# Optimization experiments

Hardware: AMD Instinct MI355X
Metric: run time of the kernel (lower is better)

Reference implementation:

```python
import jax, jax.numpy as jnp
import numpy as np

B, M, N, K = 8192, 512, 2048, 16
P = 50      # top-k support size per iteration
EPS = 0.01


def soft_threshold(x, theta, p):
    # x: [B, N]
    if p == 0:
        return jnp.sign(x) * jax.nn.relu(jnp.abs(x) - theta)
    abs_ = jnp.abs(x)
    topk_vals, _ = jax.lax.top_k(abs_, p)          # sorted descending
    thresh = topk_vals[:, -1]                      # min of top-k, per row
    keep = (abs_ > thresh[:, None]).astype(x.dtype)
    shrunk = jnp.sign(x) * jax.nn.relu(abs_ - theta)
    return keep * x + (1.0 - keep) * shrunk


def setup_inputs() -> dict:
    key = jax.random.key(0)
    k_y, k_A = jax.random.split(key)
    y = jax.random.normal(k_y, (B, M), dtype=jnp.float32)
    A = jax.random.normal(k_A, (M, N), dtype=jnp.float32) / np.sqrt(M)
    gamma = jnp.full((K,), 3.0, dtype=jnp.float32)
    theta = jnp.full((K,), 0.02, dtype=jnp.float32)
    a_param = jnp.full((K,), 0.01, dtype=jnp.float32)
    v = jnp.ones((K,), dtype=jnp.float32)
    vu = jnp.full((K,), 0.05, dtype=jnp.float32)
    theta_init = jnp.float32(1.0)
    return {"y": y, "A": A, "gamma": gamma, "theta": theta,
            "a_param": a_param, "v": v, "vu": vu,
            "theta_init": theta_init, "info": 0}


def reference(y, A, gamma, theta, a_param, v, vu, theta_init, info):
    # forward_op(x)  = x @ A.T   : [B,N] -> [B,M]
    # backward_op(b) = b @ A     : [B,M] -> [B,N]
    x = jnp.zeros((y.shape[0], A.shape[1]), dtype=y.dtype)
    for i in range(K):
        t = theta_init if i == 0 else theta[i]
        gain = 1.0 + t * vu[i] * jnp.exp(-v[i] * jnp.abs(x))
        b = (gain * x) @ A.T - y                 # residual in measurement space
        c = b @ A                                # gradient step direction
        x_new = soft_threshold(x - gamma[i] * c, theta[i], P)
        overshoot = 1.0 + a_param[i] / (jnp.abs(x_new - x) + EPS)
        x = overshoot * x_new + (1.0 - overshoot) * x
    return (x, jnp.zeros((K, 1), dtype=y.dtype), jnp.zeros((K, 1), dtype=y.dtype))
```

## Files before the change

kernel.cpp:

```cpp
#include <hip/hip_runtime.h>
#include <math.h>

#define Bsz  8192
#define Mdim 512
#define Ndim 2048
#define Kit  16
#define Pk   50
#define EPSv 0.01f

typedef __attribute__((ext_vector_type(8))) short bf16x8;
typedef __attribute__((ext_vector_type(4))) float f32x4;

static __device__ __forceinline__ unsigned short f2bf(float f) {
    unsigned u = __float_as_uint(f);
    return (unsigned short)((u + 0x7fffu + ((u >> 16) & 1u)) >> 16);
}
static __device__ __forceinline__ float bf2f(unsigned short h) {
    return __uint_as_float(((unsigned)h) << 16);
}

static __device__ __forceinline__ void gl16(const void* g, void* l) {
    __builtin_amdgcn_global_load_lds(
        (const __attribute__((address_space(1))) unsigned int*)g,
        (__attribute__((address_space(3))) unsigned int*)l, 16, 0, 0);
}

#define PIPE_BARRIER() __builtin_amdgcn_s_barrier()

#define MFMA3(acc_, bh_, bl_, ah_, al_)                                         \
    acc_ = __builtin_amdgcn_mfma_f32_16x16x32_bf16(bh_, ah_, acc_, 0, 0, 0);    \
    acc_ = __builtin_amdgcn_mfma_f32_16x16x32_bf16(bh_, al_, acc_, 0, 0, 0);    \
    acc_ = __builtin_amdgcn_mfma_f32_16x16x32_bf16(bl_, ah_, acc_, 0, 0, 0);

__global__ __launch_bounds__(256) void presplit_A(
    const float* __restrict__ A, unsigned short* __restrict__ Ah,
    unsigned short* __restrict__ Al, unsigned short* __restrict__ AhT,
    unsigned short* __restrict__ AlT)
{
    int idx = blockIdx.x * 256 + threadIdx.x;
    int m = idx >> 11, n = idx & (Ndim - 1);
    float a = A[idx];
    unsigned short h = f2bf(a);
    unsigned short l = f2bf(a - bf2f(h));
    Ah[idx] = h; Al[idx] = l;
    AhT[(size_t)n * Mdim + m] = h;
    AlT[(size_t)n * Mdim + m] = l;
}

__global__ __launch_bounds__(256) void split_negy_kernel(const float* __restrict__ y,
                                                         unsigned short* __restrict__ bS) {
    int i = blockIdx.x * 256 + threadIdx.x;
    float4 v = ((const float4*)y)[i];
    int idx = i * 4;
    int r = idx >> 9, c = idx & 511;
    float f0 = -v.x, f1 = -v.y, f2 = -v.z, f3 = -v.w;
    unsigned short h0 = f2bf(f0), h1 = f2bf(f1), h2 = f2bf(f2), h3 = f2bf(f3);
    ushort4 hv = make_ushort4(h0, h1, h2, h3);
    ushort4 lv = make_ushort4(f2bf(f0 - bf2f(h0)), f2bf(f1 - bf2f(h1)),
                              f2bf(f2 - bf2f(h2)), f2bf(f3 - bf2f(h3)));
    *(ushort4*)(bS + (size_t)r * 1024 + c)       = hv;
    *(ushort4*)(bS + (size_t)r * 1024 + 512 + c) = lv;
}

__global__ __launch_bounds__(512, 2) void gemm1_mfma(
    const unsigned short* __restrict__ zS,
    const unsigned short* __restrict__ Ah, const unsigned short* __restrict__ Al,
    const float* __restrict__ y, unsigned short* __restrict__ bS)
{
    enum { NT = 32 };
    const int tid  = threadIdx.x;
    const int lane = tid & 63, w = tid >> 6;
    const int lm   = lane & 15, quad = lane >> 4;
    const int g    = w >> 2;
    const int wg   = w & 3;
    const int wrow = (wg >> 1) * 64;
    const int wcol = (wg & 1) * 64;

    int d   = blockIdx.y * gridDim.x + blockIdx.x;
    int sid = (d & 7) * 32 + (d >> 3);
    const int m0 = (sid & 3) * 128, r0 = (sid >> 2) * 128;

    __shared__ __attribute__((aligned(16))) unsigned short smem[2 * 32768];

    f32x4 acc[4][4];
#pragma unroll
    for (int i = 0; i < 4; i++)
#pragma unroll
        for (int j = 0; j < 4; j++) acc[i][j] = (f32x4)0.f;

    const unsigned short *zhp[2], *zlp[2], *ahp[2], *alp[2]; int doff[2];
#pragma unroll
    for (int s = 0; s < 2; s++) {
        int off = ((wg * 2 + s) << 10) + lane * 16;
        int row = off >> 6;
        int kb  = (off & 63) ^ (((row >> 1) & 3) << 4);
        doff[s] = (wg * 2 + s) << 10;
        int kbase = g * 1024 + (kb >> 1);
        zhp[s]  = zS + (size_t)(r0 + row) * 4096 + kbase;
        zlp[s]  = zS + (size_t)(r0 + row) * 4096 + 2048 + kbase;
        ahp[s]  = Ah + (size_t)(m0 + row) * 2048 + kbase;
        alp[s]  = Al + (size_t)(m0 + row) * 2048 + kbase;
    }

    const int X   = ((lm >> 1) & 3) << 4;
    const int cbx = (quad * 16) ^ X;

    auto STAGE = [&](int t) {
        char* base = (char*)smem + (t & 1) * 65536 + g * 32768;
        const int ko = t * 32;
#pragma unroll
        for (int s = 0; s < 2; s++) {
            gl16(zhp[s] + ko, base +     0 + doff[s]);
            gl16(zlp[s] + ko, base +  8192 + doff[s]);
            gl16(ahp[s] + ko, base + 16384 + doff[s]);
            gl16(alp[s] + ko, base + 24576 + doff[s]);
        }
    };

    STAGE(0);
    asm volatile("s_waitcnt vmcnt(0)" ::: "memory");
    PIPE_BARRIER();

#pragma unroll 2
    for (int t = 0; t < NT; ++t) {
        const char* B0  = (const char*)smem + (t & 1) * 65536 + g * 32768;
        const char* zhB = B0, *zlB = B0 + 8192;
        const char* ahB = B0 + 16384, *alB = B0 + 24576;

        bf16x8 ahf[4], alf[4], zhf[2], zlf[2];
#pragma unroll
        for (int fj = 0; fj < 4; fj++) {
            int ar = wcol + fj * 16 + lm;
            ahf[fj] = *(const bf16x8*)(ahB + ar * 64 + cbx);
            alf[fj] = *(const bf16x8*)(alB + ar * 64 + cbx);
        }
#pragma unroll
        for (int fi = 0; fi < 2; fi++) {
            int zr = wrow + fi * 16 + lm;
            zhf[fi] = *(const bf16x8*)(zhB + zr * 64 + cbx);
            zlf[fi] = *(const bf16x8*)(zlB + zr * 64 + cbx);
        }
        if (t + 1 < NT) STAGE(t + 1);
        PIPE_BARRIER();
        asm volatile("s_waitcnt lgkmcnt(0)" ::: "memory");
        __builtin_amdgcn_sched_barrier(0);
        __builtin_amdgcn_s_setprio(1);
#pragma unroll
        for (int fi = 0; fi < 2; fi++)
#pragma unroll
            for (int fj = 0; fj < 4; fj++) {
                MFMA3(acc[fi][fj], zhf[fi], zlf[fi], ahf[fj], alf[fj]);
            }
        __builtin_amdgcn_s_setprio(0);
        PIPE_BARRIER();

#pragma unroll
        for (int fi = 0; fi < 2; fi++) {
            int zr = wrow + (fi + 2) * 16 + lm;
            zhf[fi] = *(const bf16x8*)(zhB + zr * 64 + cbx);
            zlf[fi] = *(const bf16x8*)(zlB + zr * 64 + cbx);
        }
        PIPE_BARRIER();
        asm volatile("s_waitcnt lgkmcnt(0)" ::: "memory");
        __builtin_amdgcn_sched_barrier(0);
        __builtin_amdgcn_s_setprio(1);
#pragma unroll
        for (int fi = 0; fi < 2; fi++)
#pragma unroll
            for (int fj = 0; fj < 4; fj++) {
                MFMA3(acc[fi + 2][fj], zhf[fi], zlf[fi], ahf[fj], alf[fj]);
            }
        __builtin_amdgcn_s_setprio(0);
        asm volatile("s_waitcnt vmcnt(0)" ::: "memory");
        PIPE_BARRIER();
    }

    float* cmb = (float*)smem;
    __syncthreads();
    if (g == 1) {
#pragma unroll
        for (int fi = 0; fi < 4; fi++)
#pragma unroll
            for (int fj = 0; fj < 4; fj++)
#pragma unroll
                for (int r = 0; r < 4; r++) {
                    int row = wrow + fi * 16 + quad * 4 + r;
                    int col = wcol + fj * 16 + lm;
                    cmb[row * 132 + col] = acc[fi][fj][r];
                }
    }
    __syncthreads();
    if (g == 0) {
#pragma unroll
        for (int fi = 0; fi < 4; fi++)
#pragma unroll
            for (int fj = 0; fj < 4; fj++)
#pragma unroll
                for (int r = 0; r < 4; r++) {
                    int row = wrow + fi * 16 + quad * 4 + r;
                    int col = wcol + fj * 16 + lm;
                    float bv = acc[fi][fj][r] + cmb[row * 132 + col]
                             - y[(size_t)(r0 + row) * Mdim + (m0 + col)];
                    unsigned short h = f2bf(bv);
                    bS[(size_t)(r0 + row) * 1024 + (m0 + col)]       = h;
                    bS[(size_t)(r0 + row) * 1024 + 512 + (m0 + col)] = f2bf(bv - bf2f(h));
                }
    }
}

__global__ __launch_bounds__(512, 2) void gemm2_mfma(
    const unsigned short* __restrict__ bS,
    const unsigned short* __restrict__ AhT, const unsigned short* __restrict__ AlT,
    float* __restrict__ c)
{
    enum { NT = 16 };
    const int tid  = threadIdx.x;
    const int lane = tid & 63, w = tid >> 6;
    const int lm   = lane & 15, quad = lane >> 4;
    const int wrow = (w >> 2) * 128;
    const int wcol = (w & 3) * 64;

    int d   = blockIdx.y * gridDim.x + blockIdx.x;
    int sid = (d & 7) * 32 + (d >> 3);
    const int n0 = (sid & 7) * 256, r0 = (sid >> 3) * 256;

    __shared__ __attribute__((aligned(16))) unsigned short smem[2 * 32768];

    f32x4 acc[8][4];
#pragma unroll
    for (int i = 0; i < 8; i++)
#pragma unroll
        for (int j = 0; j < 4; j++) acc[i][j] = (f32x4)0.f;

    const unsigned short *bhp[2], *blp[2], *ahp[2], *alp[2]; int doff[2];
#pragma unroll
    for (int s = 0; s < 2; s++) {
        int off = ((w * 2 + s) << 10) + lane * 16;
        int row = off >> 6;
        int kb  = (off & 63) ^ (((row >> 1) & 3) << 4);
        doff[s] = (w * 2 + s) << 10;
        bhp[s]  = bS  + (size_t)(r0 + row) * 1024 + (kb >> 1);
        blp[s]  = bS  + (size_t)(r0 + row) * 1024 + 512 + (kb >> 1);
        ahp[s]  = AhT + (size_t)(n0 + row) * 512 + (kb >> 1);
        alp[s]  = AlT + (size_t)(n0 + row) * 512 + (kb >> 1);
    }

    const int X   = ((lm >> 1) & 3) << 4;
    const int cbx = (quad * 16) ^ X;

    auto STAGE = [&](int t) {
        char* base = (char*)smem + (t & 1) * 65536;
        const int ko = t * 32;
#pragma unroll
        for (int s = 0; s < 2; s++) {
            gl16(bhp[s] + ko, base +     0 + doff[s]);
            gl16(blp[s] + ko, base + 16384 + doff[s]);
            gl16(ahp[s] + ko, base + 32768 + doff[s]);
            gl16(alp[s] + ko, base + 49152 + doff[s]);
        }
    };

    STAGE(0);
    asm volatile("s_waitcnt vmcnt(0)" ::: "memory");
    PIPE_BARRIER();

#pragma unroll 2
    for (int t = 0; t < NT; ++t) {
        const char* B0  = (const char*)smem + (t & 1) * 65536;
        const char* bhB = B0, *blB = B0 + 16384;
        const char* ahB = B0 + 32768, *alB = B0 + 49152;

        bf16x8 ahf[4], alf[4], bhf[4], blf[4];
#pragma unroll
        for (int fj = 0; fj < 4; fj++) {
            int ar = wcol + fj * 16 + lm;
            ahf[fj] = *(const bf16x8*)(ahB + ar * 64 + cbx);
            alf[fj] = *(const bf16x8*)(alB + ar * 64 + cbx);
        }
#pragma unroll
        for (int fi = 0; fi < 4; fi++) {
            int br = wrow + fi * 16 + lm;
            bhf[fi] = *(const bf16x8*)(bhB + br * 64 + cbx);
            blf[fi] = *(const bf16x8*)(blB + br * 64 + cbx);
        }
        if (t + 1 < NT) STAGE(t + 1);
        PIPE_BARRIER();
        asm volatile("s_waitcnt lgkmcnt(0)" ::: "memory");
        __builtin_amdgcn_sched_barrier(0);
        __builtin_amdgcn_s_setprio(1);
#pragma unroll
        for (int fi = 0; fi < 4; fi++)
#pragma unroll
            for (int fj = 0; fj < 4; fj++) {
                MFMA3(acc[fi][fj], bhf[fi], blf[fi], ahf[fj], alf[fj]);
            }
        __builtin_amdgcn_s_setprio(0);
        PIPE_BARRIER();

#pragma unroll
        for (int fi = 0; fi < 4; fi++) {
            int br = wrow + (fi + 4) * 16 + lm;
            bhf[fi] = *(const bf16x8*)(bhB + br * 64 + cbx);
            blf[fi] = *(const bf16x8*)(blB + br * 64 + cbx);
        }
        PIPE_BARRIER();
        asm volatile("s_waitcnt lgkmcnt(0)" ::: "memory");
        __builtin_amdgcn_sched_barrier(0);
        __builtin_amdgcn_s_setprio(1);
#pragma unroll
        for (int fi = 0; fi < 4; fi++)
#pragma unroll
            for (int fj = 0; fj < 4; fj++) {
                MFMA3(acc[fi + 4][fj], bhf[fi], blf[fi], ahf[fj], alf[fj]);
            }
        __builtin_amdgcn_s_setprio(0);
        asm volatile("s_waitcnt vmcnt(0)" ::: "memory");
        PIPE_BARRIER();
    }

#pragma unroll
    for (int fi = 0; fi < 8; fi++)
#pragma unroll
        for (int fj = 0; fj < 4; fj++)
#pragma unroll
            for (int r = 0; r < 4; r++) {
                int row = r0 + wrow + fi * 16 + quad * 4 + r;
                int col = n0 + wcol + fj * 16 + lm;
                c[(size_t)row * Ndim + col] = acc[fi][fj][r];
            }
}

__global__ __launch_bounds__(256) void topk_update_kernel(
    float* __restrict__ uz, float* __restrict__ x,
    const float* __restrict__ gamma, const float* __restrict__ theta,
    const float* __restrict__ a_param, const float* __restrict__ vv,
    const float* __restrict__ vu, int it)
{
    const int row = blockIdx.x;
    const int t   = threadIdx.x;
    float* crow = uz + (size_t)row * Ndim;
    float* xrow = x  + (size_t)row * Ndim;
    const float g = gamma[it];

    float4 c0 = *(const float4*)(crow + 4 * t);
    float4 c1 = *(const float4*)(crow + 4 * t + 1024);
    float4 x0 = *(const float4*)(xrow + 4 * t);
    float4 x1 = *(const float4*)(xrow + 4 * t + 1024);
    float cv[8] = { c0.x, c0.y, c0.z, c0.w, c1.x, c1.y, c1.z, c1.w };
    float xv[8] = { x0.x, x0.y, x0.z, x0.w, x1.x, x1.y, x1.z, x1.w };

    float uvals[8];
    unsigned keys[8];
#pragma unroll
    for (int e = 0; e < 8; e++) {
        uvals[e] = xv[e] - g * cv[e];
        keys[e]  = __float_as_uint(fabsf(uvals[e]));
    }

    __shared__ unsigned bins[2048];
    __shared__ unsigned sel[2];
    __shared__ unsigned wsum[4];

    unsigned prefix = 0;
    unsigned k = Pk;
#pragma unroll
    for (int pass = 0; pass < 3; ++pass) {
        const int      shift  = (pass == 0) ? 20 : (pass == 1) ? 9 : 0;
        const unsigned cmask  = (pass == 2) ? 511u : 2047u;
        const unsigned himask = (pass == 0) ? 0u
                              : (pass == 1) ? (0xFFFFFFFFu << 20)
                                            : (0xFFFFFFFFu << 9);
        uint4 zz = { 0u, 0u, 0u, 0u };
        ((uint4*)bins)[t]       = zz;
        ((uint4*)bins)[t + 256] = zz;
        __syncthreads();
#pragma unroll
        for (int e = 0; e < 8; e++) {
            if ((keys[e] & himask) == prefix)
                atomicAdd(&bins[(keys[e] >> shift) & cmask], 1u);
        }
        __syncthreads();
        const int base = 2040 - 8 * t;
        uint4 q0 = *(const uint4*)&bins[base];
        uint4 q1 = *(const uint4*)&bins[base + 4];
        unsigned s  = q0.x + q0.y + q0.z + q0.w + q1.x + q1.y + q1.z + q1.w;
        unsigned sc = s;
        const int ln = t & 63;
#pragma unroll
        for (int off = 1; off < 64; off <<= 1) {
            unsigned o = __shfl_up(sc, (unsigned)off);
            if (ln >= off) sc += o;
        }
        if (ln == 63) wsum[t >> 6] = sc;
        __syncthreads();
        unsigned wpre = 0;
#pragma unroll
        for (int ww = 0; ww < 3; ww++)
            if (ww < (t >> 6)) wpre += wsum[ww];
        unsigned pre = wpre + sc - s;
        if (pre < k && pre + s >= k) {
            unsigned vals[8] = { q1.w, q1.z, q1.y, q1.x, q0.w, q0.z, q0.y, q0.x };
            unsigned p2 = pre;
#pragma unroll
            for (int j = 0; j < 8; j++) {
                unsigned cb = vals[j];
                if (p2 < k && p2 + cb >= k) { sel[0] = (unsigned)(base + 7 - j); sel[1] = k - p2; }
                p2 += cb;
            }
        }
        __syncthreads();
        prefix |= sel[0] << shift;
        k = sel[1];
    }
    const float thresh = __uint_as_float(prefix);

    const float th = theta[it];
    const float ap = a_param[it];
    const bool haveNext = (it + 1) < Kit;
    float tn = 0.f, vn = 0.f, vun = 0.f;
    if (haveNext) { tn = theta[it + 1]; vn = vv[it + 1]; vun = vu[it + 1]; }

    float xo[8];
    unsigned short zh8[8], zl8[8];
#pragma unroll
    for (int e = 0; e < 8; e++) {
        float uval = uvals[e];
        float au   = fabsf(uval);
        bool keep  = au > thresh;
        float shr  = copysignf(fmaxf(au - th, 0.f), uval);
        float xn   = keep ? uval : shr;
        float dlt  = xn - xv[e];
        float ov   = 1.f + ap / (fabsf(dlt) + EPSv);
        float xr   = xv[e] + ov * dlt;
        xo[e] = xr;
        float z = (1.f + tn * vun * __expf(-vn * fabsf(xr))) * xr;
        unsigned short h = f2bf(z);
        zh8[e] = h;
        zl8[e] = f2bf(z - bf2f(h));
    }
    float4 a0 = { xo[0], xo[1], xo[2], xo[3] };
    float4 a1 = { xo[4], xo[5], xo[6], xo[7] };
    *(float4*)(xrow + 4 * t) = a0;
    *(float4*)(xrow + 4 * t + 1024) = a1;
    if (haveNext) {
        unsigned short* zp = (unsigned short*)crow;
        *(ushort4*)(zp + 4 * t)        = make_ushort4(zh8[0], zh8[1], zh8[2], zh8[3]);
        *(ushort4*)(zp + 1024 + 4 * t) = make_ushort4(zh8[4], zh8[5], zh8[6], zh8[7]);
        *(ushort4*)(zp + 2048 + 4 * t) = make_ushort4(zl8[0], zl8[1], zl8[2], zl8[3]);
        *(ushort4*)(zp + 3072 + 4 * t) = make_ushort4(zl8[4], zl8[5], zl8[6], zl8[7]);
    }
}

extern "C" void kernel_launch(void* const* d_in, const int* in_sizes, int n_in,
                              void* d_out, int out_size, void* d_ws, size_t ws_size,
                              hipStream_t stream) {
    const float* y       = (const float*)d_in[0];
    const float* A       = (const float*)d_in[1];
    const float* gamma   = (const float*)d_in[2];
    const float* theta   = (const float*)d_in[3];
    const float* a_param = (const float*)d_in[4];
    const float* v       = (const float*)d_in[5];
    const float* vu      = (const float*)d_in[6];

    float* x = (float*)d_out;

    char* ws = (char*)d_ws;
    float*          uz = (float*)ws;
    unsigned short* bS = (unsigned short*)(ws + (size_t)Bsz * Ndim * 4);
    unsigned short* Ah = (unsigned short*)(ws + (size_t)80 * 1024 * 1024);
    unsigned short* Al  = Ah  + (size_t)Mdim * Ndim;
    unsigned short* AhT = Al  + (size_t)Mdim * Ndim;
    unsigned short* AlT = AhT + (size_t)Mdim * Ndim;

    hipMemsetAsync(d_out, 0, (size_t)out_size * sizeof(float), stream);

    dim3 g1(Mdim / 128, Bsz / 128);
    dim3 g2(Ndim / 256, Bsz / 256);

    presplit_A<<<(Mdim * Ndim) / 256, dim3(256), 0, stream>>>(A, Ah, Al, AhT, AlT);
    split_negy_kernel<<<(Bsz * Mdim / 4) / 256, dim3(256), 0, stream>>>(y, bS);

    for (int it = 0; it < Kit; ++it) {
        if (it > 0)
            gemm1_mfma<<<g1, dim3(512), 0, stream>>>((const unsigned short*)uz, Ah, Al, y, bS);
        gemm2_mfma<<<g2, dim3(512), 0, stream>>>(bS, AhT, AlT, uz);
        topk_update_kernel<<<Bsz, dim3(256), 0, stream>>>(uz, x, gamma, theta, a_param, v, vu, it);
    }
}
```

Before: 2.424 ms.

## Software-pipeline LDS fragment loads across MFMA phases in both GEMM kernels

Restructures the main loops of both split-bf16 GEMM kernels so the LDS fragment reads for the next half-tile or next K-step are issued before the current MFMA block runs. This replaces the old pattern of load, barrier, wait, then compute. Barriers per K-step drop from four to one, and the explicit lgkmcnt waits are removed, so LDS latency can hide behind MFMA work. The cost is more live fragment registers (double-buffered A and B/Z fragments), which may raise VGPR pressure, and a correctness dependence on compiler-inserted waits and on the single barrier ordering buffer reuse.

```diff
diff --git a/kernel.cpp b/kernel.cpp
--- a/kernel.cpp
+++ b/kernel.cpp
@@ -27,10 +27,12 @@
 
 #define PIPE_BARRIER() __builtin_amdgcn_s_barrier()
 
-#define MFMA3(acc_, bh_, bl_, ah_, al_)                                         \
-    acc_ = __builtin_amdgcn_mfma_f32_16x16x32_bf16(bh_, ah_, acc_, 0, 0, 0);    \
-    acc_ = __builtin_amdgcn_mfma_f32_16x16x32_bf16(bh_, al_, acc_, 0, 0, 0);    \
-    acc_ = __builtin_amdgcn_mfma_f32_16x16x32_bf16(bl_, ah_, acc_, 0, 0, 0);
+#define MFMA3(acc_, bh_, bl_, ah_, al_)                                           \
+    do {                                                                          \
+        acc_ = __builtin_amdgcn_mfma_f32_16x16x32_bf16(bh_, ah_, acc_, 0, 0, 0);  \
+        acc_ = __builtin_amdgcn_mfma_f32_16x16x32_bf16(bh_, al_, acc_, 0, 0, 0);  \
+        acc_ = __builtin_amdgcn_mfma_f32_16x16x32_bf16(bl_, ah_, acc_, 0, 0, 0);  \
+    } while (0)
 
 __global__ __launch_bounds__(256) void presplit_A(
     const float* __restrict__ A, unsigned short* __restrict__ Ah,
@@ -117,62 +119,97 @@
         }
     };
 
+    auto BUF = [&](int t) -> const char* {
+        return (const char*)smem + (t & 1) * 65536 + g * 32768;
+    };
+    auto LD_A = [&](const char* B0, bf16x8 (&ah)[4], bf16x8 (&al)[4]) {
+        const char* ahB = B0 + 16384; const char* alB = B0 + 24576;
+#pragma unroll
+        for (int fj = 0; fj < 4; fj++) {
+            int ar = wcol + fj * 16 + lm;
+            ah[fj] = *(const bf16x8*)(ahB + ar * 64 + cbx);
+            al[fj] = *(const bf16x8*)(alB + ar * 64 + cbx);
+        }
+    };
+    auto LD_Z = [&](const char* B0, int rbase, bf16x8 (&zh)[2], bf16x8 (&zl)[2]) {
+        const char* zhB = B0; const char* zlB = B0 + 8192;
+#pragma unroll
+        for (int fi = 0; fi < 2; fi++) {
+            int zr = wrow + (rbase + fi) * 16 + lm;
+            zh[fi] = *(const bf16x8*)(zhB + zr * 64 + cbx);
+            zl[fi] = *(const bf16x8*)(zlB + zr * 64 + cbx);
+        }
+    };
+
+    bf16x8 ahE[4], alE[4], ahO[4], alO[4];
+    bf16x8 z01h[2], z01l[2], z23h[2], z23l[2];
+
     STAGE(0);
     asm volatile("s_waitcnt vmcnt(0)" ::: "memory");
     PIPE_BARRIER();
-
-#pragma unroll 2
-    for (int t = 0; t < NT; ++t) {
-        const char* B0  = (const char*)smem + (t & 1) * 65536 + g * 32768;
-        const char* zhB = B0, *zlB = B0 + 8192;
-        const char* ahB = B0 + 16384, *alB = B0 + 24576;
-
-        bf16x8 ahf[4], alf[4], zhf[2], zlf[2];
-#pragma unroll
-        for (int fj = 0; fj < 4; fj++) {
-            int ar = wcol + fj * 16 + lm;
-            ahf[fj] = *(const bf16x8*)(ahB + ar * 64 + cbx);
-            alf[fj] = *(const bf16x8*)(alB + ar * 64 + cbx);
-        }
+    LD_Z(BUF(0), 0, z01h, z01l);
+    LD_A(BUF(0), ahE, alE);
+
+    for (int t = 0; t < NT; t += 2) {
+        STAGE(t + 1);
+        LD_Z(BUF(t), 2, z23h, z23l);
+        __builtin_amdgcn_sched_barrier(0);
+        __builtin_amdgcn_s_setprio(1);
 #pragma unroll
         for (int fi = 0; fi < 2; fi++) {
-            int zr = wrow + fi * 16 + lm;
-            zhf[fi] = *(const bf16x8*)(zhB + zr * 64 + cbx);
-            zlf[fi] = *(const bf16x8*)(zlB + zr * 64 + cbx);
-        }
-        if (t + 1 < NT) STAGE(t + 1);
-        PIPE_BARRIER();
-        asm volatile("s_waitcnt lgkmcnt(0)" ::: "memory");
-        __builtin_amdgcn_sched_barrier(0);
-        __builtin_amdgcn_s_setprio(1);
-#pragma unroll
-        for (int fi = 0; fi < 2; fi++)
 #pragma unroll
             for (int fj = 0; fj < 4; fj++) {
-                MFMA3(acc[fi][fj], zhf[fi], zlf[fi], ahf[fj], alf[fj]);
-            }
+                MFMA3(acc[fi][fj], z01h[fi], z01l[fi], ahE[fj], alE[fj]);
+            }
+        }
         __builtin_amdgcn_s_setprio(0);
-        PIPE_BARRIER();
-
-#pragma unroll
-        for (int fi = 0; fi < 2; fi++) {
-            int zr = wrow + (fi + 2) * 16 + lm;
-            zhf[fi] = *(const bf16x8*)(zhB + zr * 64 + cbx);
-            zlf[fi] = *(const bf16x8*)(zlB + zr * 64 + cbx);
-        }
-        PIPE_BARRIER();
-        asm volatile("s_waitcnt lgkmcnt(0)" ::: "memory");
-        __builtin_amdgcn_sched_barrier(0);
-        __builtin_amdgcn_s_setprio(1);
-#pragma unroll
-        for (int fi = 0; fi < 2; fi++)
-#pragma unroll
-            for (int fj = 0; fj < 4; fj++) {
-                MFMA3(acc[fi + 2][fj], zhf[fi], zlf[fi], ahf[fj], alf[fj]);
-            }
-        __builtin_amdgcn_s_setprio(0);
+        __builtin_amdgcn_sched_barrier(0);
         asm volatile("s_waitcnt vmcnt(0)" ::: "memory");
         PIPE_BARRIER();
+        LD_Z(BUF(t + 1), 0, z01h, z01l);
+        LD_A(BUF(t + 1), ahO, alO);
+        __builtin_amdgcn_sched_barrier(0);
+        __builtin_amdgcn_s_setprio(1);
+#pragma unroll
+        for (int fi = 0; fi < 2; fi++) {
+#pragma unroll
+            for (int fj = 0; fj < 4; fj++) {
+                MFMA3(acc[fi + 2][fj], z23h[fi], z23l[fi], ahE[fj], alE[fj]);
+            }
+        }
+        __builtin_amdgcn_s_setprio(0);
+        __builtin_amdgcn_sched_barrier(0);
+
+        if (t + 2 < NT) STAGE(t + 2);
+        LD_Z(BUF(t + 1), 2, z23h, z23l);
+        __builtin_amdgcn_sched_barrier(0);
+        __builtin_amdgcn_s_setprio(1);
+#pragma unroll
+        for (int fi = 0; fi < 2; fi++) {
+#pragma unroll
+            for (int fj = 0; fj < 4; fj++) {
+                MFMA3(acc[fi][fj], z01h[fi], z01l[fi], ahO[fj], alO[fj]);
+            }
+        }
+        __builtin_amdgcn_s_setprio(0);
+        __builtin_amdgcn_sched_barrier(0);
+        asm volatile("s_waitcnt vmcnt(0)" ::: "memory");
+        PIPE_BARRIER();
+        if (t + 2 < NT) {
+            LD_Z(BUF(t + 2), 0, z01h, z01l);
+            LD_A(BUF(t + 2), ahE, alE);
+        }
+        __builtin_amdgcn_sched_barrier(0);
+        __builtin_amdgcn_s_setprio(1);
+#pragma unroll
+        for (int fi = 0; fi < 2; fi++) {
+#pragma unroll
+            for (int fj = 0; fj < 4; fj++) {
+                MFMA3(acc[fi + 2][fj], z23h[fi], z23l[fi], ahO[fj], alO[fj]);
+            }
+        }
+        __builtin_amdgcn_s_setprio(0);
+        __builtin_amdgcn_sched_barrier(0);
     }
 
     float* cmb = (float*)smem;
@@ -260,62 +297,65 @@
         }
     };
 
+    auto BUF = [&](int t) -> const char* {
+        return (const char*)smem + (t & 1) * 65536;
+    };
+    auto LD_A = [&](const char* B0, bf16x8 (&ah)[4], bf16x8 (&al)[4]) {
+        const char* ahB = B0 + 32768; const char* alB = B0 + 49152;
+#pragma unroll
+        for (int fj = 0; fj < 4; fj++) {
+            int ar = wcol + fj * 16 + lm;
+            ah[fj] = *(const bf16x8*)(ahB + ar * 64 + cbx);
+            al[fj] = *(const bf16x8*)(alB + ar * 64 + cbx);
+        }
+    };
+    auto LD_B = [&](const char* B0, int rbase, bf16x8 (&bh)[4], bf16x8 (&bl)[4]) {
+        const char* bhB = B0; const char* blB = B0 + 16384;
+#pragma unroll
+        for (int fi = 0; fi < 4; fi++) {
+            int br = wrow + (rbase + fi) * 16 + lm;
+            bh[fi] = *(const bf16x8*)(bhB + br * 64 + cbx);
+            bl[fi] = *(const bf16x8*)(blB + br * 64 + cbx);
+        }
+    };
+
+    bf16x8 ahf[4], alf[4], b03h[4], b03l[4], b47h[4], b47l[4];
+
     STAGE(0);
     asm volatile("s_waitcnt vmcnt(0)" ::: "memory");
     PIPE_BARRIER();
-
-#pragma unroll 2
+    LD_B(BUF(0), 0, b03h, b03l);
+
     for (int t = 0; t < NT; ++t) {
-        const char* B0  = (const char*)smem + (t & 1) * 65536;
-        const char* bhB = B0, *blB = B0 + 16384;
-        const char* ahB = B0 + 32768, *alB = B0 + 49152;
-
-        bf16x8 ahf[4], alf[4], bhf[4], blf[4];
-#pragma unroll
-        for (int fj = 0; fj < 4; fj++) {
-            int ar = wcol + fj * 16 + lm;
-            ahf[fj] = *(const bf16x8*)(ahB + ar * 64 + cbx);
-            alf[fj] = *(const bf16x8*)(alB + ar * 64 + cbx);
-        }
+        const char* B0 = BUF(t);
+        if (t + 1 < NT) STAGE(t + 1);
+        LD_A(B0, ahf, alf);
+        LD_B(B0, 4, b47h, b47l);
+        __builtin_amdgcn_sched_barrier(0);
+        __builtin_amdgcn_s_setprio(1);
 #pragma unroll
         for (int fi = 0; fi < 4; fi++) {
-            int br = wrow + fi * 16 + lm;
-            bhf[fi] = *(const bf16x8*)(bhB + br * 64 + cbx);
-            blf[fi] = *(const bf16x8*)(blB + br * 64 + cbx);
-        }
-        if (t + 1 < NT) STAGE(t + 1);
-        PIPE_BARRIER();
-        asm volatile("s_waitcnt lgkmcnt(0)" ::: "memory");
-        __builtin_amdgcn_sched_barrier(0);
-        __builtin_amdgcn_s_setprio(1);
-#pragma unroll
-        for (int fi = 0; fi < 4; fi++)
 #pragma unroll
             for (int fj = 0; fj < 4; fj++) {
-                MFMA3(acc[fi][fj], bhf[fi], blf[fi], ahf[fj], alf[fj]);
-            }
+                MFMA3(acc[fi][fj], b03h[fi], b03l[fi], ahf[fj], alf[fj]);
+            }
+        }
         __builtin_amdgcn_s_setprio(0);
-        PIPE_BARRIER();
-
-#pragma unroll
-        for (int fi = 0; fi < 4; fi++) {
-            int br = wrow + (fi + 4) * 16 + lm;
-            bhf[fi] = *(const bf16x8*)(bhB + br * 64 + cbx);
-            blf[fi] = *(const bf16x8*)(blB + br * 64 + cbx);
-        }
-        PIPE_BARRIER();
-        asm volatile("s_waitcnt lgkmcnt(0)" ::: "memory");
-        __builtin_amdgcn_sched_barrier(0);
-        __builtin_amdgcn_s_setprio(1);
-#pragma unroll
-        for (int fi = 0; fi < 4; fi++)
-#pragma unroll
-            for (int fj = 0; fj < 4; fj++) {
-                MFMA3(acc[fi + 4][fj], bhf[fi], blf[fi], ahf[fj], alf[fj]);
-            }
-        __builtin_amdgcn_s_setprio(0);
+        __builtin_amdgcn_sched_barrier(0);
         asm volatile("s_waitcnt vmcnt(0)" ::: "memory");
         PIPE_BARRIER();
+        if (t + 1 < NT) LD_B(BUF(t + 1), 0, b03h, b03l);
+        __builtin_amdgcn_sched_barrier(0);
+        __builtin_amdgcn_s_setprio(1);
+#pragma unroll
+        for (int fi = 0; fi < 4; fi++) {
+#pragma unroll
+            for (int fj = 0; fj < 4; fj++) {
+                MFMA3(acc[fi + 4][fj], b47h[fi], b47l[fi], ahf[fj], alf[fj]);
+            }
+        }
+        __builtin_amdgcn_s_setprio(0);
+        __builtin_amdgcn_sched_barrier(0);
     }
 
 #pragma unroll
```

After: 2.300 ms. -5.1%, faster.
